# Optimization experiments

Hardware: AMD Instinct MI355X
Metric: run time of the kernel (lower is better)

The kernel has to match this reference:

```python
import jax, jax.numpy as jnp
import numpy as np

N, CIN, H, W = 4, 1024, 96, 96
RED = 2
CINT = CIN // RED          # 512
D = 4                       # corr_disp / max_displacement
Q = (2 * D + 1) ** 2        # 81 displacement channels


def conv1x1(z, w, b):
    # z: [N,C,H,W], w: [O,C], b: [O]
    return jnp.einsum('nchw,oc->nohw', z, w) + b[None, :, None, None]


def setup_inputs() -> dict:
    key = jax.random.key(0)
    ks = jax.random.split(key, 10)
    std = 0.01
    inp = {
        'x': jax.random.normal(ks[0], (N, CIN, H, W), jnp.float32),
        'x_ref': jax.random.normal(ks[1], (N, CIN, H, W), jnp.float32),
        'w_g': jax.random.normal(ks[2], (CINT, CIN), jnp.float32) * std,
        'b_g': jnp.zeros((CINT,), jnp.float32),
        'w_theta': jax.random.normal(ks[3], (CINT, CIN), jnp.float32) * std,
        'b_theta': jnp.zeros((CINT,), jnp.float32),
        'w_phi': jax.random.normal(ks[4], (CINT, CIN), jnp.float32) * std,
        'b_phi': jnp.zeros((CINT,), jnp.float32),
        'w_out': jax.random.normal(ks[5], (CIN, CINT), jnp.float32) * std,
        'b_out': jnp.zeros((CIN,), jnp.float32),
    }
    return inp


def reference(x, x_ref, w_g, b_g, w_theta, b_theta, w_phi, b_phi, w_out, b_out):
    g = conv1x1(x_ref, w_g, b_g)          # ref value  [N,CINT,H,W]
    theta = conv1x1(x, w_theta, b_theta)  # query      [N,CINT,H,W]
    phi = conv1x1(x_ref, w_phi, b_phi)    # ref key    [N,CINT,H,W]

    # MxCorrelation (kernel=1, pad=max_disp=D): per-displacement channel dot
    # product, normalized by channel count (MXNet sumelems = 1*1*C).
    phi_pad = jnp.pad(phi, ((0, 0), (0, 0), (D, D), (D, D)))
    inv_c = jnp.float32(1.0 / CINT)
    corrs = []
    for dy in range(2 * D + 1):
        for dx in range(2 * D + 1):
            corrs.append(jnp.sum(theta * phi_pad[:, :, dy:dy + H, dx:dx + W], axis=1) * inv_c)
    pw = jnp.stack(corrs, axis=1)  # [N,Q,H,W]

    # embedded_gaussian scaling: *= 256; /= sqrt(theta_x.shape[-1]) (width!)
    pw = pw * jnp.float32(256.0 / np.sqrt(W))
    pw = jax.nn.softmax(pw, axis=1)

    # MxAssemble(k=D): gather-weighted assembly over the displacement window.
    g_pad = jnp.pad(g, ((0, 0), (0, 0), (D, D), (D, D)))
    y = jnp.zeros_like(g)
    q = 0
    for dy in range(2 * D + 1):
        for dx in range(2 * D + 1):
            y = y + pw[:, q, None, :, :] * g_pad[:, :, dy:dy + H, dx:dx + W]
            q += 1

    return x + conv1x1(y, w_out, b_out)
```

## Files before the change

### kernel.cpp

```cpp
#include <hip/hip_runtime.h>
#include <hip/hip_bf16.h>

typedef unsigned short u16;
typedef unsigned int   u32;
typedef unsigned long long uptr;
typedef short bf16x8 __attribute__((ext_vector_type(8)));
typedef float f32x4  __attribute__((ext_vector_type(4)));

#define PIMG 9216
#define HH 96
#define WW 96
#define SCALE 0.05103103630798288f

__device__ __forceinline__ u16 f2b(float f) {
  u32 u = __float_as_uint(f);
  u += 0x7fffu + ((u >> 16) & 1u);
  return (u16)(u >> 16);
}

__device__ __forceinline__ void gl2lds16(const void* g, void* l) {
  __builtin_amdgcn_global_load_lds(
      (const __attribute__((address_space(1))) void*)(uptr)g,
      (__attribute__((address_space(3))) void*)(uptr)l, 16, 0, 0);
}

__global__ void __launch_bounds__(256)
transpose_cvt(const float* __restrict__ src, u16* __restrict__ dst) {
  __shared__ float tile[64][33];
  const int tx = threadIdx.x, ty = threadIdx.y;
  const int p0 = blockIdx.x * 32, c0 = blockIdx.y * 64;
  const float* s = src + (size_t)blockIdx.z * 1024 * PIMG;
  u16* d = dst + (size_t)blockIdx.z * PIMG * 1024;
#pragma unroll
  for (int i = 0; i < 8; ++i) {
    int c = ty + i * 8;
    tile[c][tx] = s[(size_t)(c0 + c) * PIMG + p0 + tx];
  }
  __syncthreads();
#pragma unroll
  for (int i = 0; i < 4; ++i) {
    int p = ty + i * 8;
    u32 lo = f2b(tile[2 * tx][p]);
    u32 hi = f2b(tile[2 * tx + 1][p]);
    *(u32*)(d + (size_t)(p0 + p) * 1024 + c0 + 2 * tx) = lo | (hi << 16);
  }
}

__global__ void __launch_bounds__(256)
cvt_pairs(const float* __restrict__ s, u16* __restrict__ d, int n2) {
  int i = blockIdx.x * blockDim.x + threadIdx.x;
  if (i < n2) {
    float2 v = ((const float2*)s)[i];
    ((u32*)d)[i] = (u32)f2b(v.x) | ((u32)f2b(v.y) << 16);
  }
}

__global__ void zero1k(u32* z) { z[threadIdx.x] = 0; }

template <int EPI>
__global__ void __launch_bounds__(256)
gemm_bf16(const u16* __restrict__ A, const u16* __restrict__ B, int K,
          u16* __restrict__ outb, int ldo,
          const float* __restrict__ bias0, const float* __restrict__ bias1,
          int split, float* __restrict__ outf, const float* __restrict__ xres) {
  __shared__ u16 lds[2 * 128 * 64];
  u16* Alds = lds;
  u16* Blds = lds + 128 * 64;

  const int tid = threadIdx.x;
  const int wave = tid >> 6, lane = tid & 63;
  const int quad = lane >> 4, col = lane & 15;
  const int wr = wave >> 1, wc = wave & 1;

  const int nbx = gridDim.x;
  const int nwg = nbx * gridDim.y;
  const int id = blockIdx.x + nbx * blockIdx.y;
  const int nid = (id & 7) * (nwg >> 3) + (id >> 3);
  const int m0 = (nid / nbx) * 128, n0 = (nid % nbx) * 128;

  f32x4 acc[4][4] = {};

  int srow[4], skc[4];
#pragma unroll
  for (int i = 0; i < 4; ++i) {
    int c = i * 256 + tid;
    srow[i] = c >> 3;
    skc[i] = (c & 7) ^ (srow[i] & 7);
  }

  for (int k0 = 0; k0 < K; k0 += 64) {
    __syncthreads();
#pragma unroll
    for (int i = 0; i < 4; ++i)
      gl2lds16(A + (size_t)(m0 + srow[i]) * K + k0 + skc[i] * 8,
               Alds + (i * 256 + wave * 64) * 8);
#pragma unroll
    for (int i = 0; i < 4; ++i)
      gl2lds16(B + (size_t)(n0 + srow[i]) * K + k0 + skc[i] * 8,
               Blds + (i * 256 + wave * 64) * 8);
    __syncthreads();
#pragma unroll
    for (int ks = 0; ks < 2; ++ks) {
      bf16x8 af[4], bfr[4];
#pragma unroll
      for (int mt = 0; mt < 4; ++mt) {
        int row = wr * 64 + mt * 16 + col;
        int pos = (ks * 4 + quad) ^ (row & 7);
        af[mt] = *(const bf16x8*)(Alds + row * 64 + pos * 8);
      }
#pragma unroll
      for (int nt = 0; nt < 4; ++nt) {
        int row = wc * 64 + nt * 16 + col;
        int pos = (ks * 4 + quad) ^ (row & 7);
        bfr[nt] = *(const bf16x8*)(Blds + row * 64 + pos * 8);
      }
#pragma unroll
      for (int mt = 0; mt < 4; ++mt)
#pragma unroll
        for (int nt = 0; nt < 4; ++nt)
          acc[mt][nt] = __builtin_amdgcn_mfma_f32_16x16x32_bf16(
              af[mt], bfr[nt], acc[mt][nt], 0, 0, 0);
    }
  }

  if (EPI == 0) {
#pragma unroll
    for (int nt = 0; nt < 4; ++nt) {
      int n = n0 + wc * 64 + nt * 16 + col;
      float bv = (n < split) ? bias0[n] : bias1[n - split];
#pragma unroll
      for (int mt = 0; mt < 4; ++mt) {
        int mb = m0 + wr * 64 + mt * 16 + quad * 4;
#pragma unroll
        for (int r = 0; r < 4; ++r)
          outb[(size_t)(mb + r) * ldo + n] = f2b(acc[mt][nt][r] + bv);
      }
    }
  } else {
    int b = m0 / PIMG;
    int pb = m0 - b * PIMG + wr * 64;
    const float* xr = xres + (size_t)b * 1024 * PIMG;
    float* op = outf + (size_t)b * 1024 * PIMG;
#pragma unroll
    for (int nt = 0; nt < 4; ++nt) {
      int n = n0 + wc * 64 + nt * 16 + col;
      float bv = bias0[n];
#pragma unroll
      for (int mt = 0; mt < 4; ++mt) {
        int p = pb + mt * 16 + quad * 4;
        const float4 xv = *(const float4*)(xr + (size_t)n * PIMG + p);
        float4 o;
        o.x = acc[mt][nt][0] + bv + xv.x;
        o.y = acc[mt][nt][1] + bv + xv.y;
        o.z = acc[mt][nt][2] + bv + xv.z;
        o.w = acc[mt][nt][3] + bv + xv.w;
        *(float4*)(op + (size_t)n * PIMG + p) = o;
      }
    }
  }
}

__global__ void __launch_bounds__(256)
corr_mfma(const u16* __restrict__ theta, const u16* __restrict__ gphi,
          float* __restrict__ scores, const u16* __restrict__ zpage) {
  __shared__ u16 tlds[64 * 64];
  __shared__ u16 plds[256 * 64];
  const int tid = threadIdx.x;
  const int wave = tid >> 6, lane = tid & 63;
  const int quad = lane >> 4, col = lane & 15;
  const int h0 = blockIdx.y * 8, w0 = blockIdx.x * 8;
  const int pb = blockIdx.z * PIMG;

  const u16* tsrc[2];
#pragma unroll
  for (int i = 0; i < 2; ++i) {
    int u = i * 256 + tid;
    int row = u >> 3, c = u & 7;
    int p = pb + (h0 + (row >> 3)) * 96 + w0 + (row & 7);
    tsrc[i] = theta + (size_t)p * 512 + ((c ^ (row & 7)) * 8);
  }
  const u16* psrc[8];
#pragma unroll
  for (int i = 0; i < 8; ++i) {
    int u = i * 256 + tid;
    int row = u >> 3, c = u & 7;
    int hh = h0 - 4 + (row >> 4), w2 = w0 - 4 + (row & 15);
    const u16* s = ((unsigned)hh < 96u && (unsigned)w2 < 96u)
        ? gphi + (size_t)(pb + hh * 96 + w2) * 1024 + 512 : zpage;
    psrc[i] = s + ((c ^ (row & 7)) * 8);
  }

  f32x4 acc[4][4] = {};
  for (int k0 = 0; k0 < 512; k0 += 64) {
    __syncthreads();
#pragma unroll
    for (int i = 0; i < 2; ++i)
      gl2lds16(tsrc[i] + k0, tlds + (i * 256 + wave * 64) * 8);
#pragma unroll
    for (int i = 0; i < 8; ++i)
      gl2lds16(psrc[i] + k0, plds + (i * 256 + wave * 64) * 8);
    __syncthreads();
#pragma unroll
    for (int ks = 0; ks < 2; ++ks) {
      bf16x8 af[4], bfr[4];
#pragma unroll
      for (int mt = 0; mt < 4; ++mt) {
        int row = mt * 16 + col;
        int pos = (ks * 4 + quad) ^ (row & 7);
        af[mt] = *(const bf16x8*)(tlds + row * 64 + pos * 8);
      }
#pragma unroll
      for (int nt = 0; nt < 4; ++nt) {
        int row = (wave * 4 + nt) * 16 + col;
        int pos = (ks * 4 + quad) ^ (row & 7);
        bfr[nt] = *(const bf16x8*)(plds + row * 64 + pos * 8);
      }
#pragma unroll
      for (int mt = 0; mt < 4; ++mt)
#pragma unroll
        for (int nt = 0; nt < 4; ++nt)
          acc[mt][nt] = __builtin_amdgcn_mfma_f32_16x16x32_bf16(
              af[mt], bfr[nt], acc[mt][nt], 0, 0, 0);
    }
  }

#pragma unroll
  for (int nt = 0; nt < 4; ++nt) {
    int ny = wave * 4 + nt;
#pragma unroll
    for (int mt = 0; mt < 4; ++mt) {
#pragma unroll
      for (int r = 0; r < 4; ++r) {
        int m = mt * 16 + quad * 4 + r;
        int py = m >> 3, pxl = m & 7;
        int a = ny - py, b = col - pxl;
        if ((unsigned)a <= 8u && (unsigned)b <= 8u) {
          int p = pb + (h0 + py) * 96 + w0 + pxl;
          scores[(size_t)p * 81 + a * 9 + b] = acc[mt][nt][r] * SCALE;
        }
      }
    }
  }
}

__global__ void __launch_bounds__(256)
assemble3(const float* __restrict__ scores, const u16* __restrict__ gphi,
          u16* __restrict__ y) {
  __shared__ u16 smem[64 * 256];
  const int tid = threadIdx.x;
  const int wave = tid >> 6, lane = tid & 63;
  const int quad = lane >> 4, col = lane & 15;
  const int h0 = blockIdx.y * 8, w0 = blockIdx.x * 8;
  const int pb = blockIdx.z * PIMG;

  {
    uint4 z4 = make_uint4(0, 0, 0, 0);
#pragma unroll
    for (int i = 0; i < 8; ++i)
      *(uint4*)(smem + (tid * 8 + i) * 8) = z4;
  }
  __syncthreads();

  {
    const int m = tid >> 2, part = tid & 3;
    const int py = m >> 3, px = m & 7;
    const float* srow = scores + (size_t)(pb + (h0 + py) * 96 + w0 + px) * 81;
    float s[21];
    float mx = -1e30f;
#pragma unroll
    for (int i = 0; i < 21; ++i) {
      int q = part + 4 * i;
      s[i] = (q < 81) ? srow[q] : -1e30f;
      mx = fmaxf(mx, s[i]);
    }
    mx = fmaxf(mx, __shfl_xor(mx, 1));
    mx = fmaxf(mx, __shfl_xor(mx, 2));
    float sum = 0.f;
#pragma unroll
    for (int i = 0; i < 21; ++i) {
      int q = part + 4 * i;
      float e = (q < 81) ? __expf(s[i] - mx) : 0.f;
      s[i] = e;
      sum += e;
    }
    sum += __shfl_xor(sum, 1);
    sum += __shfl_xor(sum, 2);
    float inv = 1.0f / sum;
#pragma unroll
    for (int i = 0; i < 21; ++i) {
      int q = part + 4 * i;
      if (q < 81) {
        int a = q / 9, b = q - a * 9;
        int n = (py + a) * 16 + px + b;
        int addr = m * 256 + (((n >> 3) ^ (m & 7)) << 3) + (n & 7);
        smem[addr] = f2b(s[i] * inv);
      }
    }
  }
  __syncthreads();

  bf16x8 af[8];
  {
    int m = wave * 16 + col;
#pragma unroll
    for (int ks = 0; ks < 8; ++ks) {
      int c = (ks * 4 + quad) ^ (m & 7);
      af[ks] = *(const bf16x8*)(smem + m * 256 + c * 8);
    }
  }
  __syncthreads();

  int prow[4];
#pragma unroll
  for (int r = 0; r < 4; ++r) {
    int m = wave * 16 + quad * 4 + r;
    prow[r] = pb + (h0 + (m >> 3)) * 96 + w0 + (m & 7);
  }

  const int gp = tid & 31, cg = tid >> 5;
  const int hh = h0 - 4 + (gp >> 1);
  const int wb = w0 - 4 + (gp & 1) * 8;
  const bool vrow = (unsigned)hh < 96u;
  const u16* src[8];
  bool ok[8];
#pragma unroll
  for (int i = 0; i < 8; ++i) {
    int wwi = wb + i;
    ok[i] = vrow && ((unsigned)wwi < 96u);
    src[i] = gphi + (size_t)(pb + hh * 96 + wwi) * 1024 + cg * 8;
  }

  for (int c0 = 0; c0 < 512; c0 += 64) {
    uint4 v[8];
#pragma unroll
    for (int i = 0; i < 8; ++i) {
      uint4 t4 = make_uint4(0, 0, 0, 0);
      if (ok[i]) t4 = *(const uint4*)(src[i] + c0);
      v[i] = t4;
    }
    __syncthreads();
#pragma unroll
    for (int j = 0; j < 8; ++j) {
      int sw = j >> 1;
      u32 x0 = ((const u32*)&v[0])[sw], x1 = ((const u32*)&v[1])[sw];
      u32 x2 = ((const u32*)&v[2])[sw], x3 = ((const u32*)&v[3])[sw];
      u32 x4 = ((const u32*)&v[4])[sw], x5 = ((const u32*)&v[5])[sw];
      u32 x6 = ((const u32*)&v[6])[sw], x7 = ((const u32*)&v[7])[sw];
      uint4 o;
      if (j & 1) {
        o.x = (x0 >> 16) | (x1 & 0xffff0000u);
        o.y = (x2 >> 16) | (x3 & 0xffff0000u);
        o.z = (x4 >> 16) | (x5 & 0xffff0000u);
        o.w = (x6 >> 16) | (x7 & 0xffff0000u);
      } else {
        o.x = (x0 & 0xffffu) | (x1 << 16);
        o.y = (x2 & 0xffffu) | (x3 << 16);
        o.z = (x4 & 0xffffu) | (x5 << 16);
        o.w = (x6 & 0xffffu) | (x7 << 16);
      }
      *(uint4*)(smem + (cg * 8 + j) * 256 + ((gp ^ j) << 3)) = o;
    }
    __syncthreads();

    f32x4 acc[4] = {};
#pragma unroll
    for (int ks = 0; ks < 8; ++ks) {
      bf16x8 bfr[4];
#pragma unroll
      for (int nt = 0; nt < 4; ++nt) {
        int ch = nt * 16 + col;
        int c = (ks * 4 + quad) ^ (ch & 7);
        bfr[nt] = *(const bf16x8*)(smem + ch * 256 + c * 8);
      }
#pragma unroll
      for (int nt = 0; nt < 4; ++nt)
        acc[nt] = __builtin_amdgcn_mfma_f32_16x16x32_bf16(af[ks], bfr[nt],
                                                          acc[nt], 0, 0, 0);
    }
#pragma unroll
    for (int nt = 0; nt < 4; ++nt) {
      int ch = c0 + nt * 16 + col;
#pragma unroll
      for (int r = 0; r < 4; ++r)
        y[(size_t)prow[r] * 512 + ch] = f2b(acc[nt][r]);
    }
  }
}

extern "C" void kernel_launch(void* const* d_in, const int* in_sizes, int n_in,
                              void* d_out, int out_size, void* d_ws,
                              size_t ws_size, hipStream_t stream) {
  const float* x    = (const float*)d_in[0];
  const float* xref = (const float*)d_in[1];
  const float* w_g  = (const float*)d_in[2];
  const float* b_g  = (const float*)d_in[3];
  const float* w_th = (const float*)d_in[4];
  const float* b_th = (const float*)d_in[5];
  const float* w_ph = (const float*)d_in[6];
  const float* b_ph = (const float*)d_in[7];
  const float* w_o  = (const float*)d_in[8];
  const float* b_o  = (const float*)d_in[9];

  char* ws = (char*)d_ws;
  u16*   big    = (u16*)(ws);
  u16*   gphi   = (u16*)(ws + 75497472);
  u16*   theta  = (u16*)(ws + 150994944);
  float* scores = (float*)(ws + 188743680);
  u16*   wgp    = (u16*)(ws + 200687616);
  u16*   wth    = (u16*)(ws + 202784768);
  u16*   wout   = (u16*)(ws + 203833344);
  u16*   zpage  = big + 24 * 1024 * 1024;

  cvt_pairs<<<1024, 256, 0, stream>>>(w_g, wgp, 262144);
  cvt_pairs<<<1024, 256, 0, stream>>>(w_ph, wgp + 524288, 262144);
  cvt_pairs<<<1024, 256, 0, stream>>>(w_th, wth, 262144);
  cvt_pairs<<<1024, 256, 0, stream>>>(w_o, wout, 262144);

  dim3 tb(32, 8);
  transpose_cvt<<<dim3(288, 16, 4), tb, 0, stream>>>(xref, big);
  gemm_bf16<0><<<dim3(8, 288), 256, 0, stream>>>(big, wgp, 1024, gphi, 1024,
                                                 b_g, b_ph, 512, nullptr,
                                                 nullptr);
  transpose_cvt<<<dim3(288, 16, 4), tb, 0, stream>>>(x, big);
  gemm_bf16<0><<<dim3(4, 288), 256, 0, stream>>>(big, wth, 1024, theta, 512,
                                                 b_th, b_th, 512, nullptr,
                                                 nullptr);

  zero1k<<<1, 256, 0, stream>>>((u32*)zpage);

  corr_mfma<<<dim3(12, 12, 4), 256, 0, stream>>>(theta, gphi, scores, zpage);
  assemble3<<<dim3(12, 12, 4), 256, 0, stream>>>(scores, gphi, big );

  gemm_bf16<1><<<dim3(8, 288), 256, 0, stream>>>(big, wout, 512, nullptr, 0,
                                                 b_o, b_o, 1024, (float*)d_out,
                                                 x);
}
```

Before: 726.8 us.

## Rewrite GEMM as 256x128 tile with triple-buffered async LDS pipeline

Replaces the 128x128 double-sync GEMM with a 512-thread 256x128 tile kernel. A three-stage LDS ring is filled by global_load_lds, with prefetch two tiles ahead interleaved among the MFMA groups and vmcnt-based waits replacing the paired __syncthreads. It also raises wave priority around MFMA bursts. The aim is to hide global load latency and improve operand reuse, at the cost of more LDS (72KB) per block, which may reduce occupancy.

```diff
diff --git a/kernel.cpp b/kernel.cpp
--- a/kernel.cpp
+++ b/kernel.cpp
@@ -57,80 +57,121 @@
 
 __global__ void zero1k(u32* z) { z[threadIdx.x] = 0; }
 
+#define BUFSZ (256 * 64 + 128 * 64)
+
 template <int EPI>
-__global__ void __launch_bounds__(256)
-gemm_bf16(const u16* __restrict__ A, const u16* __restrict__ B, int K,
-          u16* __restrict__ outb, int ldo,
-          const float* __restrict__ bias0, const float* __restrict__ bias1,
-          int split, float* __restrict__ outf, const float* __restrict__ xres) {
-  __shared__ u16 lds[2 * 128 * 64];
-  u16* Alds = lds;
-  u16* Blds = lds + 128 * 64;
+__global__ void __launch_bounds__(512)
+gemm256(const u16* __restrict__ A, const u16* __restrict__ B, int K,
+        u16* __restrict__ outb, int ldo,
+        const float* __restrict__ bias0, const float* __restrict__ bias1,
+        int split, float* __restrict__ outf, const float* __restrict__ xres) {
+  __shared__ __attribute__((aligned(16))) u16 lds[3 * BUFSZ];
 
   const int tid = threadIdx.x;
   const int wave = tid >> 6, lane = tid & 63;
   const int quad = lane >> 4, col = lane & 15;
-  const int wr = wave >> 1, wc = wave & 1;
+  const int wr = wave >> 2, wc = wave & 3;
 
   const int nbx = gridDim.x;
   const int nwg = nbx * gridDim.y;
   const int id = blockIdx.x + nbx * blockIdx.y;
   const int nid = (id & 7) * (nwg >> 3) + (id >> 3);
-  const int m0 = (nid / nbx) * 128, n0 = (nid % nbx) * 128;
-
-  f32x4 acc[4][4] = {};
-
-  int srow[4], skc[4];
+  const int m0 = (nid / nbx) * 256, n0 = (nid % nbx) * 128;
+
+  f32x4 acc[8][2] = {};
+
+  int arow[4], akc[4];
 #pragma unroll
   for (int i = 0; i < 4; ++i) {
-    int c = i * 256 + tid;
-    srow[i] = c >> 3;
-    skc[i] = (c & 7) ^ (srow[i] & 7);
-  }
-
-  for (int k0 = 0; k0 < K; k0 += 64) {
-    __syncthreads();
-#pragma unroll
-    for (int i = 0; i < 4; ++i)
-      gl2lds16(A + (size_t)(m0 + srow[i]) * K + k0 + skc[i] * 8,
-               Alds + (i * 256 + wave * 64) * 8);
-#pragma unroll
-    for (int i = 0; i < 4; ++i)
-      gl2lds16(B + (size_t)(n0 + srow[i]) * K + k0 + skc[i] * 8,
-               Blds + (i * 256 + wave * 64) * 8);
-    __syncthreads();
-#pragma unroll
-    for (int ks = 0; ks < 2; ++ks) {
-      bf16x8 af[4], bfr[4];
-#pragma unroll
-      for (int mt = 0; mt < 4; ++mt) {
-        int row = wr * 64 + mt * 16 + col;
+    int u = i * 512 + tid;
+    arow[i] = u >> 3;
+    akc[i] = (u & 7) ^ (arow[i] & 7);
+  }
+  int brow[2], bkc[2];
+#pragma unroll
+  for (int i = 0; i < 2; ++i) {
+    int u = i * 512 + tid;
+    brow[i] = u >> 3;
+    bkc[i] = (u & 7) ^ (brow[i] & 7);
+  }
+
+  const int NT = K >> 6;
+
+#define STAGE_A(t, i)                                                      \
+  gl2lds16(A + (size_t)(m0 + arow[i]) * K + (t) * 64 + akc[i] * 8,         \
+           lds + ((t) % 3) * BUFSZ + ((i) * 512 + wave * 64) * 8)
+#define STAGE_B(t, i)                                                      \
+  gl2lds16(B + (size_t)(n0 + brow[i]) * K + (t) * 64 + bkc[i] * 8,         \
+           lds + ((t) % 3) * BUFSZ + 256 * 64 + ((i) * 512 + wave * 64) * 8)
+
+  STAGE_A(0, 0); STAGE_A(0, 1); STAGE_A(0, 2); STAGE_A(0, 3);
+  STAGE_B(0, 0); STAGE_B(0, 1);
+  if (NT > 1) {
+    STAGE_A(1, 0); STAGE_A(1, 1); STAGE_A(1, 2); STAGE_A(1, 3);
+    STAGE_B(1, 0); STAGE_B(1, 1);
+  }
+
+  for (int t = 0; t < NT; ++t) {
+    if (t + 1 < NT)
+      asm volatile("s_waitcnt vmcnt(6)" ::: "memory");
+    else
+      asm volatile("s_waitcnt vmcnt(0)" ::: "memory");
+    asm volatile("s_barrier" ::: "memory");
+
+    const u16* bufA = lds + (t % 3) * BUFSZ;
+    const u16* bufB = bufA + 256 * 64;
+    const bool pf = (t + 2 < NT);
+
+    bf16x8 bfr[2][2];
+#pragma unroll
+    for (int nt = 0; nt < 2; ++nt)
+#pragma unroll
+      for (int ks = 0; ks < 2; ++ks) {
+        int row = wc * 32 + nt * 16 + col;
         int pos = (ks * 4 + quad) ^ (row & 7);
-        af[mt] = *(const bf16x8*)(Alds + row * 64 + pos * 8);
-      }
-#pragma unroll
-      for (int nt = 0; nt < 4; ++nt) {
-        int row = wc * 64 + nt * 16 + col;
-        int pos = (ks * 4 + quad) ^ (row & 7);
-        bfr[nt] = *(const bf16x8*)(Blds + row * 64 + pos * 8);
-      }
-#pragma unroll
-      for (int mt = 0; mt < 4; ++mt)
-#pragma unroll
-        for (int nt = 0; nt < 4; ++nt)
-          acc[mt][nt] = __builtin_amdgcn_mfma_f32_16x16x32_bf16(
-              af[mt], bfr[nt], acc[mt][nt], 0, 0, 0);
-    }
-  }
+        bfr[nt][ks] = *(const bf16x8*)(bufB + row * 64 + pos * 8);
+      }
+
+#pragma unroll
+    for (int q = 0; q < 4; ++q) {
+      bf16x8 af[2][2];
+#pragma unroll
+      for (int mi = 0; mi < 2; ++mi)
+#pragma unroll
+        for (int ks = 0; ks < 2; ++ks) {
+          int row = wr * 128 + (q * 2 + mi) * 16 + col;
+          int pos = (ks * 4 + quad) ^ (row & 7);
+          af[mi][ks] = *(const bf16x8*)(bufA + row * 64 + pos * 8);
+        }
+      if (pf) {
+        if (q == 0) { STAGE_A(t + 2, 0); STAGE_A(t + 2, 1); }
+        else if (q == 1) { STAGE_A(t + 2, 2); STAGE_A(t + 2, 3); }
+        else if (q == 2) { STAGE_B(t + 2, 0); }
+        else { STAGE_B(t + 2, 1); }
+      }
+      __builtin_amdgcn_s_setprio(1);
+#pragma unroll
+      for (int mi = 0; mi < 2; ++mi)
+#pragma unroll
+        for (int nt = 0; nt < 2; ++nt)
+#pragma unroll
+          for (int ks = 0; ks < 2; ++ks)
+            acc[q * 2 + mi][nt] = __builtin_amdgcn_mfma_f32_16x16x32_bf16(
+                af[mi][ks], bfr[nt][ks], acc[q * 2 + mi][nt], 0, 0, 0);
+      __builtin_amdgcn_s_setprio(0);
+    }
+  }
+#undef STAGE_A
+#undef STAGE_B
 
   if (EPI == 0) {
 #pragma unroll
-    for (int nt = 0; nt < 4; ++nt) {
-      int n = n0 + wc * 64 + nt * 16 + col;
+    for (int nt = 0; nt < 2; ++nt) {
+      int n = n0 + wc * 32 + nt * 16 + col;
       float bv = (n < split) ? bias0[n] : bias1[n - split];
 #pragma unroll
-      for (int mt = 0; mt < 4; ++mt) {
-        int mb = m0 + wr * 64 + mt * 16 + quad * 4;
+      for (int mt = 0; mt < 8; ++mt) {
+        int mb = m0 + wr * 128 + mt * 16 + quad * 4;
 #pragma unroll
         for (int r = 0; r < 4; ++r)
           outb[(size_t)(mb + r) * ldo + n] = f2b(acc[mt][nt][r] + bv);
@@ -138,15 +179,15 @@
     }
   } else {
     int b = m0 / PIMG;
-    int pb = m0 - b * PIMG + wr * 64;
+    int pb = m0 - b * PIMG + wr * 128;
     const float* xr = xres + (size_t)b * 1024 * PIMG;
     float* op = outf + (size_t)b * 1024 * PIMG;
 #pragma unroll
-    for (int nt = 0; nt < 4; ++nt) {
-      int n = n0 + wc * 64 + nt * 16 + col;
+    for (int nt = 0; nt < 2; ++nt) {
+      int n = n0 + wc * 32 + nt * 16 + col;
       float bv = bias0[n];
 #pragma unroll
-      for (int mt = 0; mt < 4; ++mt) {
+      for (int mt = 0; mt < 8; ++mt) {
         int p = pb + mt * 16 + quad * 4;
         const float4 xv = *(const float4*)(xr + (size_t)n * PIMG + p);
         float4 o;
@@ -418,20 +459,20 @@
 
   dim3 tb(32, 8);
   transpose_cvt<<<dim3(288, 16, 4), tb, 0, stream>>>(xref, big);
-  gemm_bf16<0><<<dim3(8, 288), 256, 0, stream>>>(big, wgp, 1024, gphi, 1024,
-                                                 b_g, b_ph, 512, nullptr,
-                                                 nullptr);
+  gemm256<0><<<dim3(8, 144), 512, 0, stream>>>(big, wgp, 1024, gphi, 1024,
+                                               b_g, b_ph, 512, nullptr,
+                                               nullptr);
   transpose_cvt<<<dim3(288, 16, 4), tb, 0, stream>>>(x, big);
-  gemm_bf16<0><<<dim3(4, 288), 256, 0, stream>>>(big, wth, 1024, theta, 512,
-                                                 b_th, b_th, 512, nullptr,
-                                                 nullptr);
+  gemm256<0><<<dim3(4, 144), 512, 0, stream>>>(big, wth, 1024, theta, 512,
+                                               b_th, b_th, 512, nullptr,
+                                               nullptr);
 
   zero1k<<<1, 256, 0, stream>>>((u32*)zpage);
 
   corr_mfma<<<dim3(12, 12, 4), 256, 0, stream>>>(theta, gphi, scores, zpage);
   assemble3<<<dim3(12, 12, 4), 256, 0, stream>>>(scores, gphi, big );
 
-  gemm_bf16<1><<<dim3(8, 288), 256, 0, stream>>>(big, wout, 512, nullptr, 0,
-                                                 b_o, b_o, 1024, (float*)d_out,
-                                                 x);
-}
+  gemm256<1><<<dim3(8, 144), 512, 0, stream>>>(big, wout, 512, nullptr, 0,
+                                               b_o, b_o, 1024, (float*)d_out,
+                                               x);
+}
```

Result: faster. 698.8 us (-3.8%).
